# Optimization experiments

Measured on AMD Instinct MI355X. Metric: run time of the kernel, lower is better.

Reference implementation:

```python
import jax, jax.numpy as jnp
import numpy as np

TEMPERATURE = 8.0  # d_k ** 0.5 with d_k = 64
NEG_INF = -1.0e9


def setup_inputs() -> dict:
    key = jax.random.key(0)
    kq, kk, kv, km = jax.random.split(key, 4)
    B, H, L, D = 2, 16, 2048, 64
    q = jax.random.normal(kq, (B, H, L, D), dtype=jnp.float32)
    k = jax.random.normal(kk, (B, H, L, D), dtype=jnp.float32)
    v = jax.random.normal(kv, (B, H, L, D), dtype=jnp.float32)
    mask = jax.random.randint(km, (B, 1, L, L), 0, 2, dtype=jnp.int32)
    return {"q": q, "k": k, "v": v, "mask": mask}


def reference(q, k, v, mask):
    # scores: [B, H, Lq, Lk]
    scores = jnp.einsum("bhqd,bhkd->bhqk", q / TEMPERATURE, k)
    scores = jnp.where(mask == 0, NEG_INF, scores)
    attn = jax.nn.softmax(scores, axis=-1)  # dropout is identity in eval mode
    out = jnp.einsum("bhqk,bhkd->bhqd", attn, v)
    return (out, attn)
```

## Files before the change

kernel.cpp:

```cpp
#include <hip/hip_runtime.h>

#define L_ 2048
#define D_ 64

typedef __attribute__((ext_vector_type(8))) short bf16x8;
typedef __attribute__((ext_vector_type(4))) float f32x4;
typedef __attribute__((ext_vector_type(2))) float f32x2;
typedef __attribute__((ext_vector_type(8))) _Float16 f16x8;
typedef __attribute__((ext_vector_type(2))) _Float16 f16x2;

__device__ __forceinline__ unsigned short f2bf(float x) {
  union { float f; unsigned u; } v; v.f = x;
  return (unsigned short)((v.u + 0x7fffu + ((v.u >> 16) & 1u)) >> 16);
}
__device__ __forceinline__ float bf2f(unsigned short h) {
  union { unsigned u; float f; } v; v.u = ((unsigned)h) << 16; return v.f;
}

__global__ __launch_bounds__(256) void ksplit(const float* __restrict__ k,
                                              unsigned short* __restrict__ kh,
                                              unsigned short* __restrict__ kl) {
  size_t o = ((size_t)blockIdx.x * 256 + threadIdx.x) * 8;
  #pragma unroll
  for (int j = 0; j < 8; ++j) {
    float x = k[o + j];
    unsigned short h = f2bf(x);
    kh[o + j] = h;
    kl[o + j] = f2bf(x - bf2f(h));
  }
}

__global__ __launch_bounds__(256) void vtrans(const float* __restrict__ v,
                                              _Float16* __restrict__ vt) {
  __shared__ _Float16 T[64][72];
  const int blk = blockIdx.x;
  const int bh  = blk >> 5;
  const int k0  = (blk & 31) << 6;
  const int tid = threadIdx.x;
  const float* vb = v + (size_t)bh * (L_ * D_) + (size_t)k0 * D_;
  const int r = tid >> 4, c4 = (tid & 15) << 2;
  #pragma unroll
  for (int p = 0; p < 4; ++p) {
    float4 u = *(const float4*)(vb + (size_t)(r + p * 16) * D_ + c4);
    T[r + p * 16][c4 + 0] = (_Float16)u.x;
    T[r + p * 16][c4 + 1] = (_Float16)u.y;
    T[r + p * 16][c4 + 2] = (_Float16)u.z;
    T[r + p * 16][c4 + 3] = (_Float16)u.w;
  }
  __syncthreads();
  _Float16* vo = vt + (size_t)bh * (D_ * L_);
  const int d = tid >> 2, kk = (tid & 3) << 4;
  f16x8 w0, w1;
  #pragma unroll
  for (int j = 0; j < 8; ++j) { w0[j] = T[kk + j][d]; w1[j] = T[kk + 8 + j][d]; }
  *(f16x8*)(vo + (size_t)d * L_ + k0 + kk) = w0;
  *(f16x8*)(vo + (size_t)d * L_ + k0 + kk + 8) = w1;
}

__device__ __forceinline__ void split4(const float4 u, float sc, bf16x8& h, bf16x8& l, int o) {
  float s; unsigned short hh;
  s = u.x * sc; hh = f2bf(s); h[o+0] = (short)hh; l[o+0] = (short)f2bf(s - bf2f(hh));
  s = u.y * sc; hh = f2bf(s); h[o+1] = (short)hh; l[o+1] = (short)f2bf(s - bf2f(hh));
  s = u.z * sc; hh = f2bf(s); h[o+2] = (short)hh; l[o+2] = (short)f2bf(s - bf2f(hh));
  s = u.w * sc; hh = f2bf(s); h[o+3] = (short)hh; l[o+3] = (short)f2bf(s - bf2f(hh));
}

template<bool USE_WS>
__device__ __forceinline__ void load_kfrag(const unsigned short* hpb, const unsigned short* lpb,
                                           const float* kfb, int ct,
                                           bf16x8& b0h, bf16x8& b1h, bf16x8& b0l, bf16x8& b1l) {
  if (USE_WS) {
    const unsigned short* hp = hpb + ct * (16 * D_);
    const unsigned short* lp = lpb + ct * (16 * D_);
    b0h = *(const bf16x8*)(hp);
    b1h = *(const bf16x8*)(hp + 32);
    b0l = *(const bf16x8*)(lp);
    b1l = *(const bf16x8*)(lp + 32);
  } else {
    const float* kp = kfb + ct * (16 * D_);
    #pragma unroll
    for (int j = 0; j < 4; ++j) {
      float x0 = kp[j], x1 = kp[4 + j], x2 = kp[32 + j], x3 = kp[36 + j];
      b0h[j]     = (short)f2bf(x0); b0l[j]     = (short)f2bf(x0 - bf2f((unsigned short)b0h[j]));
      b0h[4 + j] = (short)f2bf(x1); b0l[4 + j] = (short)f2bf(x1 - bf2f((unsigned short)b0h[4 + j]));
      b1h[j]     = (short)f2bf(x2); b1l[j]     = (short)f2bf(x2 - bf2f((unsigned short)b1h[j]));
      b1h[4 + j] = (short)f2bf(x3); b1l[4 + j] = (short)f2bf(x3 - bf2f((unsigned short)b1h[4 + j]));
    }
  }
}

template<bool USE_WS, bool USE_VT>
__global__ __launch_bounds__(512, 4) void attn_fused(
    const float* __restrict__ qf, const float* __restrict__ kf,
    const unsigned short* __restrict__ khp, const unsigned short* __restrict__ klp,
    const int* __restrict__ mask, const float* __restrict__ vf,
    const _Float16* __restrict__ vtp_g,
    float* __restrict__ outp, float* __restrict__ attnp) {
  __shared__ __align__(16) unsigned int Wst[8][16 * 20];
  __shared__ float Ored[8][16][66];
  __shared__ float red[16][9];
  __shared__ float rowL[16];

  const int tid  = threadIdx.x;
  const int p    = blockIdx.x;
  const int wg   = ((p & 7) << 9) | (p >> 3);
  const int bh   = wg >> 7;
  const int q0   = (wg & 127) << 4;
  const int b    = bh >> 4;
  const int lane = tid & 63;
  const int wave = tid >> 6;
  const int c16  = lane & 15;
  const int quad = lane >> 4;

  bf16x8 a0h, a0l, a1h, a1l;
  {
    const float* qp = qf + ((size_t)(bh * L_ + q0 + c16)) * D_ + (quad << 3);
    split4(*(const float4*)qp,        0.125f, a0h, a0l, 0);
    split4(*(const float4*)(qp + 4),  0.125f, a0h, a0l, 4);
    split4(*(const float4*)(qp + 32), 0.125f, a1h, a1l, 0);
    split4(*(const float4*)(qp + 36), 0.125f, a1h, a1l, 4);
  }

  const int qrow = q0 + c16;
  const int* mbase = mask + ((size_t)(b * L_) + qrow) * L_ + (wave << 8) + (quad << 2);

  const unsigned short* hpb = nullptr;
  const unsigned short* lpb = nullptr;
  const float* kfb = nullptr;
  if (USE_WS) {
    hpb = khp + (size_t)bh * (L_ * D_) + ((size_t)((wave << 8) + c16)) * D_ + (quad << 3);
    lpb = klp + (size_t)bh * (L_ * D_) + ((size_t)((wave << 8) + c16)) * D_ + (quad << 3);
  } else {
    kfb = kf + (size_t)bh * (L_ * D_) + ((size_t)((wave << 8) + c16)) * D_ + (quad << 3);
  }

  f16x2 E[32];
  float lsum = 0.f;

  #pragma unroll
  for (int ct = 0; ct < 16; ++ct) {
    bf16x8 b0h, b1h, b0l, b1l;
    load_kfrag<USE_WS>(hpb, lpb, kfb, ct, b0h, b1h, b0l, b1l);
    const int4 mk = *(const int4*)(mbase + (ct << 4));
    f32x4 acc1 = {-6.f, -6.f, -6.f, -6.f};
    f32x4 acc2 = {0.f, 0.f, 0.f, 0.f};
    __builtin_amdgcn_s_setprio(1);
    acc1 = __builtin_amdgcn_mfma_f32_16x16x32_bf16(b0h, a0h, acc1, 0, 0, 0);
    acc2 = __builtin_amdgcn_mfma_f32_16x16x32_bf16(b1h, a1h, acc2, 0, 0, 0);
    acc1 = __builtin_amdgcn_mfma_f32_16x16x32_bf16(b0l, a0h, acc1, 0, 0, 0);
    acc2 = __builtin_amdgcn_mfma_f32_16x16x32_bf16(b1l, a1h, acc2, 0, 0, 0);
    acc1 = __builtin_amdgcn_mfma_f32_16x16x32_bf16(b0h, a0l, acc1, 0, 0, 0);
    acc2 = __builtin_amdgcn_mfma_f32_16x16x32_bf16(b1h, a1l, acc2, 0, 0, 0);
    __builtin_amdgcn_s_setprio(0);
    float e0 = mk.x ? __expf(acc1[0] + acc2[0]) : 0.f;
    float e1 = mk.y ? __expf(acc1[1] + acc2[1]) : 0.f;
    float e2 = mk.z ? __expf(acc1[2] + acc2[2]) : 0.f;
    float e3 = mk.w ? __expf(acc1[3] + acc2[3]) : 0.f;
    lsum += (e0 + e1) + (e2 + e3);
    E[2 * ct]     = f16x2{(_Float16)e0, (_Float16)e1};
    E[2 * ct + 1] = f16x2{(_Float16)e2, (_Float16)e3};
  }

  lsum += __shfl_xor(lsum, 16);
  lsum += __shfl_xor(lsum, 32);
  if (lane < 16) red[lane][wave] = lsum;
  __syncthreads();
  if (tid < 16) {
    float l = 0.f;
    #pragma unroll
    for (int w = 0; w < 8; ++w) l += red[tid][w];
    rowL[tid] = (l > 0.f) ? (1.f / l) : 0.f;
  }
  __syncthreads();
  const float inv = rowL[c16];

  float* abase = attnp + ((size_t)(bh * L_) + qrow) * L_ + (wave << 8) + (quad << 2);
  unsigned int* Wp = &Wst[wave][0];
  const int wr = c16 * 20;
  const _Float16* vt0 = nullptr;
  if (USE_VT) vt0 = vtp_g + (size_t)bh * (D_ * L_) + (size_t)c16 * L_ + (wave << 8) + (quad << 3);
  f32x4 o0 = {0.f, 0.f, 0.f, 0.f}, o1 = o0, o2 = o0, o3 = o0;

  #pragma unroll
  for (int c = 0; c < 8; ++c) {
    #pragma unroll
    for (int h = 0; h < 2; ++h) {
      const int ei = (c << 2) + (h << 1);
      Wp[wr + (h << 3) + (quad << 1) + 0] = __builtin_bit_cast(unsigned int, E[ei]);
      Wp[wr + (h << 3) + (quad << 1) + 1] = __builtin_bit_cast(unsigned int, E[ei + 1]);
      f32x4 pa = { (float)E[ei][0] * inv, (float)E[ei][1] * inv,
                   (float)E[ei + 1][0] * inv, (float)E[ei + 1][1] * inv };
      __builtin_nontemporal_store(pa, (f32x4*)(abase + (c << 5) + (h << 4)));
    }
    __builtin_amdgcn_wave_barrier();
    const f16x8 A = *(const f16x8*)&Wst[wave][wr + (quad << 2)];
    __builtin_amdgcn_s_setprio(1);
    if (USE_VT) {
      o0 = __builtin_amdgcn_mfma_f32_16x16x32_f16(A, *(const f16x8*)(vt0 + (c << 5)), o0, 0, 0, 0);
      o1 = __builtin_amdgcn_mfma_f32_16x16x32_f16(A, *(const f16x8*)(vt0 + 16 * L_ + (c << 5)), o1, 0, 0, 0);
      o2 = __builtin_amdgcn_mfma_f32_16x16x32_f16(A, *(const f16x8*)(vt0 + 32 * L_ + (c << 5)), o2, 0, 0, 0);
      o3 = __builtin_amdgcn_mfma_f32_16x16x32_f16(A, *(const f16x8*)(vt0 + 48 * L_ + (c << 5)), o3, 0, 0, 0);
    } else {
      const float* vb = vf + (size_t)bh * (L_ * D_);
      const int kb = (wave << 8) + (c << 5) + (quad << 3);
      f16x8 bv0, bv1, bv2, bv3;
      #pragma unroll
      for (int j = 0; j < 8; ++j) {
        const float* vr = vb + (size_t)(kb + j) * D_ + c16;
        bv0[j] = (_Float16)vr[0];
        bv1[j] = (_Float16)vr[16];
        bv2[j] = (_Float16)vr[32];
        bv3[j] = (_Float16)vr[48];
      }
      o0 = __builtin_amdgcn_mfma_f32_16x16x32_f16(A, bv0, o0, 0, 0, 0);
      o1 = __builtin_amdgcn_mfma_f32_16x16x32_f16(A, bv1, o1, 0, 0, 0);
      o2 = __builtin_amdgcn_mfma_f32_16x16x32_f16(A, bv2, o2, 0, 0, 0);
      o3 = __builtin_amdgcn_mfma_f32_16x16x32_f16(A, bv3, o3, 0, 0, 0);
    }
    __builtin_amdgcn_s_setprio(0);
  }

  {
    const int r0 = quad << 2;
    #pragma unroll
    for (int g = 0; g < 4; ++g) {
      Ored[wave][r0 + g][c16]      = o0[g];
      Ored[wave][r0 + g][16 + c16] = o1[g];
      Ored[wave][r0 + g][32 + c16] = o2[g];
      Ored[wave][r0 + g][48 + c16] = o3[g];
    }
  }
  __syncthreads();
  {
    const int r = tid >> 5, d0 = (tid & 31) << 1;
    const float sc = rowL[r];
    f32x2 s = {0.f, 0.f};
    #pragma unroll
    for (int w = 0; w < 8; ++w) {
      s[0] += Ored[w][r][d0 + 0];
      s[1] += Ored[w][r][d0 + 1];
    }
    s[0] *= sc; s[1] *= sc;
    float* dst = outp + ((size_t)(bh * L_ + q0 + r)) * D_ + d0;
    __builtin_nontemporal_store(s, (f32x2*)dst);
  }
}

extern "C" void kernel_launch(void* const* d_in, const int* in_sizes, int n_in,
                              void* d_out, int out_size, void* d_ws, size_t ws_size,
                              hipStream_t stream) {
  const float* q = (const float*)d_in[0];
  const float* k = (const float*)d_in[1];
  const float* v = (const float*)d_in[2];
  const int* mask = (const int*)d_in[3];
  float* outp  = (float*)d_out;
  float* attnp = outp + (size_t)4194304;

  if (ws_size >= (size_t)25165824) {
    unsigned short* kh = (unsigned short*)d_ws;
    unsigned short* kl = kh + (size_t)4194304;
    _Float16* vt = (_Float16*)(kl + (size_t)4194304);
    ksplit<<<2048, 256, 0, stream>>>(k, kh, kl);
    vtrans<<<1024, 256, 0, stream>>>(v, vt);
    attn_fused<true, true><<<4096, 512, 0, stream>>>(q, k, kh, kl, mask, v, vt, outp, attnp);
  } else if (ws_size >= (size_t)16777216) {
    unsigned short* kh = (unsigned short*)d_ws;
    unsigned short* kl = kh + (size_t)4194304;
    ksplit<<<2048, 256, 0, stream>>>(k, kh, kl);
    attn_fused<true, false><<<4096, 512, 0, stream>>>(q, k, kh, kl, mask, v, nullptr, outp, attnp);
  } else {
    attn_fused<false, false><<<4096, 512, 0, stream>>>(q, k, nullptr, nullptr, mask, v, nullptr, outp, attnp);
  }
}
```

Before: 941.2 us.

## Alias staging buffer into Ored, reorder block-to-head mapping, widen output reduction stores

```diff
diff --git a/kernel.cpp b/kernel.cpp
--- a/kernel.cpp
+++ b/kernel.cpp
@@ -5,7 +5,6 @@
 
 typedef __attribute__((ext_vector_type(8))) short bf16x8;
 typedef __attribute__((ext_vector_type(4))) float f32x4;
-typedef __attribute__((ext_vector_type(2))) float f32x2;
 typedef __attribute__((ext_vector_type(8))) _Float16 f16x8;
 typedef __attribute__((ext_vector_type(2))) _Float16 f16x2;
 
@@ -96,17 +95,18 @@
     const int* __restrict__ mask, const float* __restrict__ vf,
     const _Float16* __restrict__ vtp_g,
     float* __restrict__ outp, float* __restrict__ attnp) {
-  __shared__ __align__(16) unsigned int Wst[8][16 * 20];
-  __shared__ float Ored[8][16][66];
+  __shared__ __align__(16) float Ored[8][16][66];
   __shared__ float red[16][9];
   __shared__ float rowL[16];
 
   const int tid  = threadIdx.x;
   const int p    = blockIdx.x;
-  const int wg   = ((p & 7) << 9) | (p >> 3);
-  const int bh   = wg >> 7;
-  const int q0   = (wg & 127) << 4;
-  const int b    = bh >> 4;
+  const int g    = ((p & 7) << 9) | (p >> 3);
+  const int h    = g & 15;
+  const int r_   = g >> 4;
+  const int q0   = (r_ & 127) << 4;
+  const int b    = r_ >> 7;
+  const int bh   = (b << 4) | h;
   const int lane = tid & 63;
   const int wave = tid >> 6;
   const int c16  = lane & 15;
@@ -175,7 +175,7 @@
   const float inv = rowL[c16];
 
   float* abase = attnp + ((size_t)(bh * L_) + qrow) * L_ + (wave << 8) + (quad << 2);
-  unsigned int* Wp = &Wst[wave][0];
+  unsigned int* Wp = reinterpret_cast<unsigned int*>(&Ored[0][0][0]) + wave * 320;
   const int wr = c16 * 20;
   const _Float16* vt0 = nullptr;
   if (USE_VT) vt0 = vtp_g + (size_t)bh * (D_ * L_) + (size_t)c16 * L_ + (wave << 8) + (quad << 3);
@@ -184,16 +184,16 @@
   #pragma unroll
   for (int c = 0; c < 8; ++c) {
     #pragma unroll
-    for (int h = 0; h < 2; ++h) {
-      const int ei = (c << 2) + (h << 1);
-      Wp[wr + (h << 3) + (quad << 1) + 0] = __builtin_bit_cast(unsigned int, E[ei]);
-      Wp[wr + (h << 3) + (quad << 1) + 1] = __builtin_bit_cast(unsigned int, E[ei + 1]);
+    for (int hh = 0; hh < 2; ++hh) {
+      const int ei = (c << 2) + (hh << 1);
+      Wp[wr + (hh << 3) + (quad << 1) + 0] = __builtin_bit_cast(unsigned int, E[ei]);
+      Wp[wr + (hh << 3) + (quad << 1) + 1] = __builtin_bit_cast(unsigned int, E[ei + 1]);
       f32x4 pa = { (float)E[ei][0] * inv, (float)E[ei][1] * inv,
                    (float)E[ei + 1][0] * inv, (float)E[ei + 1][1] * inv };
-      __builtin_nontemporal_store(pa, (f32x4*)(abase + (c << 5) + (h << 4)));
+      __builtin_nontemporal_store(pa, (f32x4*)(abase + (c << 5) + (hh << 4)));
     }
     __builtin_amdgcn_wave_barrier();
-    const f16x8 A = *(const f16x8*)&Wst[wave][wr + (quad << 2)];
+    const f16x8 A = *(const f16x8*)(Wp + wr + (quad << 2));
     __builtin_amdgcn_s_setprio(1);
     if (USE_VT) {
       o0 = __builtin_amdgcn_mfma_f32_16x16x32_f16(A, *(const f16x8*)(vt0 + (c << 5)), o0, 0, 0, 0);
@@ -220,29 +220,32 @@
     __builtin_amdgcn_s_setprio(0);
   }
 
+  __syncthreads();
   {
     const int r0 = quad << 2;
     #pragma unroll
-    for (int g = 0; g < 4; ++g) {
-      Ored[wave][r0 + g][c16]      = o0[g];
-      Ored[wave][r0 + g][16 + c16] = o1[g];
-      Ored[wave][r0 + g][32 + c16] = o2[g];
-      Ored[wave][r0 + g][48 + c16] = o3[g];
-    }
-  }
-  __syncthreads();
-  {
-    const int r = tid >> 5, d0 = (tid & 31) << 1;
+    for (int gI = 0; gI < 4; ++gI) {
+      Ored[wave][r0 + gI][c16]      = o0[gI];
+      Ored[wave][r0 + gI][16 + c16] = o1[gI];
+      Ored[wave][r0 + gI][32 + c16] = o2[gI];
+      Ored[wave][r0 + gI][48 + c16] = o3[gI];
+    }
+  }
+  __syncthreads();
+  if (tid < 256) {
+    const int r = tid >> 4, d0 = (tid & 15) << 2;
     const float sc = rowL[r];
-    f32x2 s = {0.f, 0.f};
+    f32x4 s = {0.f, 0.f, 0.f, 0.f};
     #pragma unroll
     for (int w = 0; w < 8; ++w) {
       s[0] += Ored[w][r][d0 + 0];
       s[1] += Ored[w][r][d0 + 1];
-    }
-    s[0] *= sc; s[1] *= sc;
+      s[2] += Ored[w][r][d0 + 2];
+      s[3] += Ored[w][r][d0 + 3];
+    }
+    s[0] *= sc; s[1] *= sc; s[2] *= sc; s[3] *= sc;
     float* dst = outp + ((size_t)(bh * L_ + q0 + r)) * D_ + d0;
-    __builtin_nontemporal_store(s, (f32x2*)dst);
+    __builtin_nontemporal_store(s, (f32x4*)dst);
   }
 }
 
```

New measurement: 969.3 us. 1.03x slower.
